# Kernel optimization log

Hardware: AMD Instinct MI355X
Metric: run time of the kernel (lower is better)

## Reference

```python
import jax, jax.numpy as jnp
import numpy as np

B, T, SD = 16, 512, 64          # batch, action seq len, sample_dim
EMB, HD = 1024, 64              # emb_dim, head_dim
NH = EMB // HD                  # 16 heads
DEPTH, NREG, LAT, FF = 8, 16, 256, 4 * EMB
S = T + NREG                    # total sequence length (actions + registers)


def setup_inputs() -> dict:
    key = jax.random.key(0)
    ks = jax.random.split(key, 16)
    def n(k, shape, scale=0.02):
        return jax.random.normal(k, shape, jnp.float32) * scale
    return {
        "sample": jax.random.normal(ks[0], (B, T, SD), jnp.float32),
        "W_emb": n(ks[1], (SD, EMB)), "b_emb": jnp.zeros((EMB,), jnp.float32),
        "pos": n(ks[2], (T, EMB)),
        "registers": n(ks[3], (NREG, EMB), 1.0),
        "ln1_s": jnp.ones((DEPTH, EMB), jnp.float32), "ln1_b": jnp.zeros((DEPTH, EMB), jnp.float32),
        "W_qkv": n(ks[4], (DEPTH, EMB, 3 * EMB)), "b_qkv": jnp.zeros((DEPTH, 3 * EMB), jnp.float32),
        "W_o": n(ks[5], (DEPTH, EMB, EMB)), "b_o": jnp.zeros((DEPTH, EMB), jnp.float32),
        "ln2_s": jnp.ones((DEPTH, EMB), jnp.float32), "ln2_b": jnp.zeros((DEPTH, EMB), jnp.float32),
        "W_fc1": n(ks[6], (DEPTH, EMB, FF)), "b_fc1": jnp.zeros((DEPTH, FF), jnp.float32),
        "W_fc2": n(ks[7], (DEPTH, FF, EMB)), "b_fc2": jnp.zeros((DEPTH, EMB), jnp.float32),
        "lnf_s": jnp.ones((EMB,), jnp.float32), "lnf_b": jnp.zeros((EMB,), jnp.float32),
        "W_head": n(ks[8], (EMB, LAT)), "b_head": jnp.zeros((LAT,), jnp.float32),
    }


def _ln(x, s, b):
    m = jnp.mean(x, -1, keepdims=True)
    v = jnp.var(x, -1, keepdims=True)
    return (x - m) * jax.lax.rsqrt(v + 1e-5) * s + b


def _causal_last_mask():
    # True = attended to. Actions attend to all actions but NOT registers;
    # registers attend to all actions and causally (incl. self) to registers.
    allowed = jnp.ones((S, S), jnp.bool_)
    allowed = allowed.at[:T, T:].set(False)
    allowed = allowed.at[T:, T:].set(jnp.tril(jnp.ones((NREG, NREG), jnp.bool_)))
    return allowed


def reference(sample, W_emb, b_emb, pos, registers, ln1_s, ln1_b, W_qkv, b_qkv,
              W_o, b_o, ln2_s, ln2_b, W_fc1, b_fc1, W_fc2, b_fc2,
              lnf_s, lnf_b, W_head, b_head):
    # embed + positional add
    x = sample @ W_emb + b_emb + pos[None, :, :]          # [B,T,E]
    # concat registers
    x = jnp.concatenate([x, jnp.broadcast_to(registers, (B, NREG, EMB))], axis=1)  # [B,S,E]
    mask = _causal_last_mask()                             # [S,S]
    scale = 1.0 / jnp.sqrt(jnp.asarray(HD, x.dtype))
    for i in range(DEPTH):
        # pre-LN multi-head attention with structured block mask
        h = _ln(x, ln1_s[i], ln1_b[i])
        qkv = h @ W_qkv[i] + b_qkv[i]
        q, k, v = jnp.split(qkv, 3, axis=-1)
        q = q.reshape(B, S, NH, HD)
        k = k.reshape(B, S, NH, HD)
        v = v.reshape(B, S, NH, HD)
        att = jnp.einsum('bqhd,bkhd->bhqk', q, k) * scale
        att = jnp.where(mask[None, None], att, jnp.finfo(att.dtype).min)
        att = jax.nn.softmax(att, axis=-1)
        o = jnp.einsum('bhqk,bkhd->bqhd', att, v).reshape(B, S, EMB)
        x = x + o @ W_o[i] + b_o[i]
        # pre-LN MLP
        h2 = _ln(x, ln2_s[i], ln2_b[i])
        x = x + jax.nn.gelu(h2 @ W_fc1[i] + b_fc1[i]) @ W_fc2[i] + b_fc2[i]
    x = _ln(x, lnf_s, lnf_b)
    # head applied to register positions only
    return x[:, T:] @ W_head + b_head                      # [B,NREG,LAT]
```

## Files before the change

kernel.cpp:

```cpp
#include <hip/hip_runtime.h>
#include <hip/hip_bf16.h>


typedef unsigned short u16;
typedef __attribute__((ext_vector_type(4))) float f32x4;
typedef __attribute__((ext_vector_type(8))) __bf16 bf16x8;

#define DEV static __device__ __forceinline__

constexpr int Bb = 16, Tt = 512, E = 1024, HD = 64, NHd = 16;
constexpr int DEPTH = 8, NREG = 16, LAT = 256, FF = 4096;
constexpr int S = Tt + NREG;
constexpr int SPAD = 576;
constexpr int MR = Bb * S;
constexpr int ME = Bb * Tt;

DEV u16 f2bf(float f) {
  unsigned u = __builtin_bit_cast(unsigned, f);
  u += 0x7fffu + ((u >> 16) & 1u);
  return (u16)(u >> 16);
}
DEV float bf2f(u16 h) { return __builtin_bit_cast(float, (unsigned)h << 16); }

DEV void gll16(const u16* g, u16* l) {
  __builtin_amdgcn_global_load_lds((const __attribute__((address_space(1))) void*)g,
                                   (__attribute__((address_space(3))) void*)l, 16, 0, 0);
}

enum { M_EMBED, M_QKV, M_OPROJ, M_FC1, M_FC2, M_HEAD };

struct GA {
  const u16* A; const u16* Bt;
  int K, lda, ldb, Nrows, ldc;
  const float* bias; const float* pos;
  float* fout; u16* bout;
  u16 *qp, *kp, *vtp;
};

template<int MODE, int BN>
__global__ __launch_bounds__(256)
void gemm_bt(GA g) {
  constexpr int NI = BN / 32;
  __shared__ __align__(16) u16 As[3][128 * 32];
  __shared__ __align__(16) u16 Bs[3][BN * 32];
  const int tid = threadIdx.x;
  const u16* A  = g.A;
  const u16* Bt = g.Bt;

  int tM, tN;
  {
    const int nwg = gridDim.x * gridDim.y;
    int flat = blockIdx.y * gridDim.x + blockIdx.x;
    const int q = nwg >> 3, r = nwg & 7;
    const int xcd = flat & 7, loc = flat >> 3;
    flat = (xcd < r ? xcd * (q + 1) : r * (q + 1) + (xcd - r) * q) + loc;
    tM = flat / gridDim.x; tN = flat % gridDim.x;
  }

  const int lane = tid & 63, wid = tid >> 6;
  const int wr = wid >> 1, wc = wid & 1;
  const int fr = lane & 15, fg = lane >> 4;

  const int arow = tM * 128 + (tid >> 2);
  int br0 = tN * BN + (tid >> 2);
  if (br0 > g.Nrows - 1) br0 = g.Nrows - 1;
  int br1 = tN * BN + 64 + (tid >> 2);
  if (br1 > g.Nrows - 1) br1 = g.Nrows - 1;
  const int kseg = ((tid & 3) ^ ((tid >> 3) & 3)) * 8;
  const int woff = (tid & 192) * 8;

  const u16* ag0 = A  + (long)arow        * g.lda + kseg;
  const u16* ag1 = A  + (long)(arow + 64) * g.lda + kseg;
  const u16* bg0 = Bt + (long)br0         * g.ldb + kseg;
  const u16* bg1 = Bt + (long)br1         * g.ldb + kseg;

  f32x4 acc[4][NI];
#pragma unroll
  for (int i = 0; i < 4; ++i)
#pragma unroll
    for (int j = 0; j < NI; ++j) acc[i][j] = f32x4{0.f, 0.f, 0.f, 0.f};

#define STAGE(KT, BUF) do {                                   \
    const int _k0 = (KT) << 5;                                \
    gll16(ag0 + _k0, &As[BUF][woff]);                         \
    gll16(ag1 + _k0, &As[BUF][woff + 2048]);                  \
    gll16(bg0 + _k0, &Bs[BUF][woff]);                         \
    if (BN == 128) gll16(bg1 + _k0, &Bs[BUF][woff + 2048]);   \
  } while (0)

  const int nk = g.K >> 5;
  STAGE(0, 0);
  if (nk > 1) STAGE(1, 1);

  const int rsw = (fg ^ ((fr >> 1) & 3)) * 8;
  constexpr int LPS = (BN == 128) ? 4 : 3;

  for (int kt = 0; kt < nk; ++kt) {
    const int cur = kt % 3;
    if (kt < nk - 1) {
      asm volatile("s_waitcnt vmcnt(%0)" :: "i"(LPS) : "memory");
    } else {
      asm volatile("s_waitcnt vmcnt(0)" ::: "memory");
    }
    __builtin_amdgcn_sched_barrier(0);
    __builtin_amdgcn_s_barrier();
    __builtin_amdgcn_sched_barrier(0);
    if (kt + 2 < nk) STAGE(kt + 2, (kt + 2) % 3);

    bf16x8 af[4], bfr[NI];
#pragma unroll
    for (int mi = 0; mi < 4; ++mi)
      af[mi] = *(const bf16x8*)&As[cur][(wr * 64 + mi * 16 + fr) * 32 + rsw];
#pragma unroll
    for (int ni = 0; ni < NI; ++ni)
      bfr[ni] = *(const bf16x8*)&Bs[cur][(wc * (BN / 2) + ni * 16 + fr) * 32 + rsw];
    __builtin_amdgcn_s_setprio(1);
#pragma unroll
    for (int mi = 0; mi < 4; ++mi)
#pragma unroll
      for (int ni = 0; ni < NI; ++ni)
        acc[mi][ni] = __builtin_amdgcn_mfma_f32_16x16x32_bf16(af[mi], bfr[ni], acc[mi][ni], 0, 0, 0);
    __builtin_amdgcn_s_setprio(0);
  }
#undef STAGE

#pragma unroll
  for (int mi = 0; mi < 4; ++mi)
#pragma unroll
    for (int ni = 0; ni < NI; ++ni)
#pragma unroll
      for (int j = 0; j < 4; ++j) {
        const int row = tM * 128 + wr * 64 + mi * 16 + fg * 4 + j;
        const int col = tN * BN + wc * (BN / 2) + ni * 16 + fr;
        float v = acc[mi][ni][j];
        if (MODE == M_EMBED) {
          const int b = row >> 9, t = row & 511;
          v += g.bias[col] + g.pos[(long)t * E + col];
          g.fout[((long)(b * S + t)) * E + col] = v;
        } else if (MODE == M_QKV) {
          const int b = row / S, s = row - b * S;
          v += g.bias[col];
          const int part = col >> 10, c = col & 1023;
          const int hh = c >> 6, d = c & 63;
          const u16 bf = f2bf(v);
          if (part == 0)      g.qp [((long)((b * NHd + hh) * SPAD + s)) * HD + d] = bf;
          else if (part == 1) g.kp [((long)((b * NHd + hh) * SPAD + s)) * HD + d] = bf;
          else                g.vtp[((long)((b * NHd + hh) * HD   + d)) * SPAD + s] = bf;
        } else if (MODE == M_OPROJ || MODE == M_FC2) {
          const long idx = (long)row * g.ldc + col;
          g.fout[idx] += v + g.bias[col];
        } else if (MODE == M_FC1) {
          v += g.bias[col];
          const float z = 0.7978845608028654f * (v + 0.044715f * v * v * v);
          const float e = __expf(2.f * z);
          const float th = 1.f - 2.f / (e + 1.f);
          g.bout[(long)row * g.ldc + col] = f2bf(0.5f * v * (1.f + th));
        } else if (MODE == M_HEAD) {
          g.fout[(long)row * g.ldc + col] = v + g.bias[col];
        }
      }
}

__global__ __launch_bounds__(256)
void flash_k(const u16* __restrict__ q, const u16* __restrict__ k,
             const u16* __restrict__ vt, u16* __restrict__ o) {
  __shared__ __align__(16) u16 Ks[2][64 * 64];
  __shared__ __align__(16) u16 Vs[2][64 * 64];
  __shared__ __align__(16) u16 Ps[4 * 32 * 64];
  const int tid = threadIdx.x;
  const int lane = tid & 63, w = tid >> 6;
  const int fr = lane & 15, fg = lane >> 4;

  int flat = blockIdx.y * 5 + blockIdx.x;
  flat = (flat & 7) * 160 + (flat >> 3);
  const int bh = flat / 5, qt = flat % 5;
  const int q0 = qt * 128;

  bf16x8 qf[2][2];
#pragma unroll
  for (int ms = 0; ms < 2; ++ms) {
    int qr = q0 + w * 32 + ms * 16 + fr;
    if (qr > SPAD - 1) qr = SPAD - 1;
    const u16* qrow = q + ((long)bh * SPAD + qr) * HD;
    qf[ms][0] = *(const bf16x8*)(qrow + fg * 8);
    qf[ms][1] = *(const bf16x8*)(qrow + 32 + fg * 8);
  }

  const int srow = lane >> 3;
  const int sseg = (((lane & 7) ^ (srow & 7)) * 8);
  const u16* kg = k  + ((long)bh * SPAD + w * 16 + srow) * HD + sseg;
  const u16* vg = vt + ((long)(bh * HD + w * 16 + srow)) * SPAD + sseg;

#define STAGE_F(KT, BUF) do {                                       \
    gll16(kg + (KT) * 64 * HD,          &Ks[BUF][w * 16 * HD]);     \
    gll16(kg + (KT) * 64 * HD + 8 * HD, &Ks[BUF][w * 16 * HD + 8 * HD]); \
    gll16(vg + (KT) * 64,               &Vs[BUF][w * 16 * HD]);     \
    gll16(vg + (KT) * 64 + 8 * SPAD,    &Vs[BUF][w * 16 * HD + 8 * HD]); \
  } while (0)

  const int frm = fr & 7;

  float m[2][4], lsum[2][4]; f32x4 oa[2][4];
#pragma unroll
  for (int ms = 0; ms < 2; ++ms)
#pragma unroll
    for (int j = 0; j < 4; ++j) { m[ms][j] = -1e30f; lsum[ms][j] = 0.f; }
#pragma unroll
  for (int ms = 0; ms < 2; ++ms)
#pragma unroll
    for (int n = 0; n < 4; ++n) oa[ms][n] = f32x4{0.f, 0.f, 0.f, 0.f};

  const int nt = (qt < 4) ? 8 : 9;
  STAGE_F(0, 0);
  for (int kt = 0; kt < nt; ++kt) {
    const int cur = kt & 1;
    asm volatile("s_waitcnt vmcnt(0)" ::: "memory");
    __builtin_amdgcn_sched_barrier(0);
    __builtin_amdgcn_s_barrier();
    __builtin_amdgcn_sched_barrier(0);
    if (kt + 1 < nt) STAGE_F(kt + 1, cur ^ 1);

    f32x4 sfr[2][4];
#pragma unroll
    for (int n = 0; n < 4; ++n) {
      const bf16x8 kf0 = *(const bf16x8*)&Ks[cur][(n * 16 + fr) * HD + ((fg ^ frm) * 8)];
      const bf16x8 kf1 = *(const bf16x8*)&Ks[cur][(n * 16 + fr) * HD + (((fg + 4) ^ frm) * 8)];
#pragma unroll
      for (int ms = 0; ms < 2; ++ms) {
        sfr[ms][n] = __builtin_amdgcn_mfma_f32_16x16x32_bf16(qf[ms][0], kf0, f32x4{0.f,0.f,0.f,0.f}, 0, 0, 0);
        sfr[ms][n] = __builtin_amdgcn_mfma_f32_16x16x32_bf16(qf[ms][1], kf1, sfr[ms][n], 0, 0, 0);
      }
    }
    float p[2][4][4];
#pragma unroll
    for (int ms = 0; ms < 2; ++ms)
#pragma unroll
      for (int j = 0; j < 4; ++j) {
        const int qg = q0 + w * 32 + ms * 16 + fg * 4 + j;
        const int vlim = qg < Tt ? Tt : qg + 1;
#pragma unroll
        for (int n = 0; n < 4; ++n) {
          const int col = kt * 64 + n * 16 + fr;
          p[ms][n][j] = (col < vlim) ? sfr[ms][n][j] * 0.125f : -1e30f;
        }
      }
#pragma unroll
    for (int ms = 0; ms < 2; ++ms)
#pragma unroll
      for (int j = 0; j < 4; ++j) {
        float pm = fmaxf(fmaxf(p[ms][0][j], p[ms][1][j]), fmaxf(p[ms][2][j], p[ms][3][j]));
#pragma unroll
        for (int msk = 1; msk <= 8; msk <<= 1) pm = fmaxf(pm, __shfl_xor(pm, msk));
        const float mn = fmaxf(m[ms][j], pm);
        const float corr = __expf(m[ms][j] - mn);
        m[ms][j] = mn;
        float rs = 0.f;
#pragma unroll
        for (int n = 0; n < 4; ++n) { const float e = __expf(p[ms][n][j] - mn); p[ms][n][j] = e; rs += e; }
#pragma unroll
        for (int msk = 1; msk <= 8; msk <<= 1) rs += __shfl_xor(rs, msk);
        lsum[ms][j] = lsum[ms][j] * corr + rs;
#pragma unroll
        for (int n = 0; n < 4; ++n) oa[ms][n][j] *= corr;
      }
#pragma unroll
    for (int ms = 0; ms < 2; ++ms)
#pragma unroll
      for (int j = 0; j < 4; ++j) {
        const int r = ms * 16 + fg * 4 + j;
#pragma unroll
        for (int n = 0; n < 4; ++n) {
          const int gr = 2 * n + (fr >> 3);
          Ps[w * 2048 + r * 64 + ((gr ^ (r & 7)) * 8) + frm] = f2bf(p[ms][n][j]);
        }
      }
    asm volatile("s_waitcnt lgkmcnt(0)" ::: "memory");
    __builtin_amdgcn_sched_barrier(0);
    bf16x8 pf[2][2];
#pragma unroll
    for (int ms = 0; ms < 2; ++ms) {
      pf[ms][0] = *(const bf16x8*)&Ps[w * 2048 + (ms * 16 + fr) * 64 + ((fg ^ frm) * 8)];
      pf[ms][1] = *(const bf16x8*)&Ps[w * 2048 + (ms * 16 + fr) * 64 + (((fg + 4) ^ frm) * 8)];
    }
#pragma unroll
    for (int n = 0; n < 4; ++n) {
      const bf16x8 vf0 = *(const bf16x8*)&Vs[cur][(n * 16 + fr) * HD + ((fg ^ frm) * 8)];
      const bf16x8 vf1 = *(const bf16x8*)&Vs[cur][(n * 16 + fr) * HD + (((fg + 4) ^ frm) * 8)];
#pragma unroll
      for (int ms = 0; ms < 2; ++ms) {
        oa[ms][n] = __builtin_amdgcn_mfma_f32_16x16x32_bf16(pf[ms][0], vf0, oa[ms][n], 0, 0, 0);
        oa[ms][n] = __builtin_amdgcn_mfma_f32_16x16x32_bf16(pf[ms][1], vf1, oa[ms][n], 0, 0, 0);
      }
    }
  }
#undef STAGE_F

  const int b = bh >> 4, hh = bh & 15;
#pragma unroll
  for (int ms = 0; ms < 2; ++ms)
#pragma unroll
    for (int j = 0; j < 4; ++j) {
      const int qg = q0 + w * 32 + ms * 16 + fg * 4 + j;
      if (qg < S) {
        const float inv = 1.f / lsum[ms][j];
#pragma unroll
        for (int n = 0; n < 4; ++n)
          o[((long)(b * S + qg)) * E + hh * HD + n * 16 + fr] = f2bf(oa[ms][n][j] * inv);
      }
    }
}

__global__ __launch_bounds__(256)
void ln_k(const float* __restrict__ x, const float* __restrict__ sc,
          const float* __restrict__ bi, u16* __restrict__ out, int gather) {
  const int r = blockIdx.x;
  const int srow = gather ? ((r >> 4) * S + Tt + (r & 15)) : r;
  const float4 v = ((const float4*)(x + (long)srow * E))[threadIdx.x];
  float s = v.x + v.y + v.z + v.w;
  float q = v.x * v.x + v.y * v.y + v.z * v.z + v.w * v.w;
#pragma unroll
  for (int o = 32; o; o >>= 1) { s += __shfl_down(s, o); q += __shfl_down(q, o); }
  __shared__ float ps[8];
  if ((threadIdx.x & 63) == 0) { ps[threadIdx.x >> 6] = s; ps[4 + (threadIdx.x >> 6)] = q; }
  __syncthreads();
  s = ps[0] + ps[1] + ps[2] + ps[3];
  q = ps[4] + ps[5] + ps[6] + ps[7];
  const float mean = s * (1.f / E);
  const float rs = rsqrtf(q * (1.f / E) - mean * mean + 1e-5f);
  const int c = threadIdx.x * 4;
  ushort4 o4;
  o4.x = f2bf((v.x - mean) * rs * sc[c + 0] + bi[c + 0]);
  o4.y = f2bf((v.y - mean) * rs * sc[c + 1] + bi[c + 1]);
  o4.z = f2bf((v.z - mean) * rs * sc[c + 2] + bi[c + 2]);
  o4.w = f2bf((v.w - mean) * rs * sc[c + 3] + bi[c + 3]);
  ((ushort4*)(out + (long)r * E))[threadIdx.x] = o4;
}

__global__ __launch_bounds__(256)
void wtrans(const float* __restrict__ src, u16* __restrict__ dst, int R, int C) {
  __shared__ float t[32][33];
  const int c0 = blockIdx.x * 32, r0 = blockIdx.y * 32;
  const int tx = threadIdx.x & 31, ty = threadIdx.x >> 5;
#pragma unroll
  for (int i = 0; i < 32; i += 8) t[ty + i][tx] = src[(long)(r0 + ty + i) * C + c0 + tx];
  __syncthreads();
#pragma unroll
  for (int i = 0; i < 32; i += 8) dst[(long)(c0 + ty + i) * R + r0 + tx] = f2bf(t[tx][ty + i]);
}

struct WT4 {
  const float* s[4]; u16* d[4];
  int R[4], C[4], tx[4], st[4];
};
__global__ __launch_bounds__(256)
void wtrans4(WT4 a) {
  const int bid = blockIdx.x;
  const int wsel = (bid >= a.st[1]) + (bid >= a.st[2]) + (bid >= a.st[3]);
  const int t = bid - a.st[wsel];
  const int c0 = (t % a.tx[wsel]) * 32, r0 = (t / a.tx[wsel]) * 32;
  const float* src = a.s[wsel]; u16* dst = a.d[wsel];
  const int R = a.R[wsel], C = a.C[wsel];
  __shared__ float tt[32][33];
  const int tx = threadIdx.x & 31, ty = threadIdx.x >> 5;
#pragma unroll
  for (int i = 0; i < 32; i += 8) tt[ty + i][tx] = src[(long)(r0 + ty + i) * C + c0 + tx];
  __syncthreads();
#pragma unroll
  for (int i = 0; i < 32; i += 8) dst[(long)(c0 + ty + i) * R + r0 + tx] = f2bf(tt[tx][ty + i]);
}

__global__ void cvt_bf(const float* __restrict__ in, u16* __restrict__ out, long n) {
  const long i = ((long)blockIdx.x * blockDim.x + threadIdx.x) * 4;
  if (i >= n) return;
  const float4 v = *(const float4*)(in + i);
  ushort4 o; o.x = f2bf(v.x); o.y = f2bf(v.y); o.z = f2bf(v.z); o.w = f2bf(v.w);
  *(ushort4*)(out + i) = o;
}

__global__ void zero_k(float4* p, long n) {
  long i = (long)blockIdx.x * blockDim.x + threadIdx.x;
  const long st = (long)gridDim.x * blockDim.x;
  const float4 z = make_float4(0.f, 0.f, 0.f, 0.f);
  for (; i < n; i += st) p[i] = z;
}

__global__ void reg_copy(const float* __restrict__ regs, float* __restrict__ x) {
  const int b = blockIdx.x >> 4, r = blockIdx.x & 15;
  const float4* sp = (const float4*)(regs + (long)r * E);
  float4* dp = (float4*)(x + ((long)(b * S + Tt + r)) * E);
  dp[threadIdx.x] = sp[threadIdx.x];
}

constexpr long OFF_WQKV = 0L;
constexpr long OFF_WO   = OFF_WQKV + 3072L * 1024 * 2;
constexpr long OFF_WFC1 = OFF_WO   + 1024L * 1024 * 2;
constexpr long OFF_WFC2 = OFF_WFC1 + 4096L * 1024 * 2;
constexpr long OFF_WEMB = OFF_WFC2 + 1024L * 4096 * 2;
constexpr long OFF_WHEAD= OFF_WEMB + 1024L * 64 * 2;
constexpr long OFF_SMP  = OFF_WHEAD+ 256L * 1024 * 2;
constexpr long OFF_X    = OFF_SMP  + (long)ME * 64 * 2;
constexpr long OFF_H    = OFF_X    + (long)MR * E * 4;
constexpr long OFF_Q    = OFF_H    + (long)MR * E * 2;
constexpr long OFF_K    = OFF_Q    + 256L * SPAD * HD * 2;
constexpr long OFF_VT   = OFF_K    + 256L * SPAD * HD * 2;
constexpr long OFF_O    = OFF_VT   + 256L * SPAD * HD * 2;
constexpr long OFF_HF   = OFF_O    + (long)MR * FF * 2;
constexpr long WS_NEED  = OFF_HF   + 256L * 1024 * 2;

extern "C" void kernel_launch(void* const* d_in, const int* in_sizes, int n_in,
                              void* d_out, int out_size, void* d_ws, size_t ws_size,
                              hipStream_t stream) {
  if (ws_size < (size_t)WS_NEED) return;

  const float* sample = (const float*)d_in[0];
  const float* W_emb  = (const float*)d_in[1];
  const float* b_emb  = (const float*)d_in[2];
  const float* pos    = (const float*)d_in[3];
  const float* regs   = (const float*)d_in[4];
  const float* ln1_s  = (const float*)d_in[5];
  const float* ln1_b  = (const float*)d_in[6];
  const float* W_qkv  = (const float*)d_in[7];
  const float* b_qkv  = (const float*)d_in[8];
  const float* W_o    = (const float*)d_in[9];
  const float* b_o    = (const float*)d_in[10];
  const float* ln2_s  = (const float*)d_in[11];
  const float* ln2_b  = (const float*)d_in[12];
  const float* W_fc1  = (const float*)d_in[13];
  const float* b_fc1  = (const float*)d_in[14];
  const float* W_fc2  = (const float*)d_in[15];
  const float* b_fc2  = (const float*)d_in[16];
  const float* lnf_s  = (const float*)d_in[17];
  const float* lnf_b  = (const float*)d_in[18];
  const float* W_head = (const float*)d_in[19];
  const float* b_head = (const float*)d_in[20];

  char* w = (char*)d_ws;
  u16* wqkvT = (u16*)(w + OFF_WQKV);
  u16* woT   = (u16*)(w + OFF_WO);
  u16* wfc1T = (u16*)(w + OFF_WFC1);
  u16* wfc2T = (u16*)(w + OFF_WFC2);
  u16* wembT = (u16*)(w + OFF_WEMB);
  u16* wheadT= (u16*)(w + OFF_WHEAD);
  u16* smp   = (u16*)(w + OFF_SMP);
  float* x   = (float*)(w + OFF_X);
  u16* h     = (u16*)(w + OFF_H);
  u16* qp    = (u16*)(w + OFF_Q);
  u16* kp    = (u16*)(w + OFF_K);
  u16* vtp   = (u16*)(w + OFF_VT);
  u16* o     = (u16*)(w + OFF_O);
  u16* a1    = (u16*)(w + OFF_O);
  u16* hf    = (u16*)(w + OFF_HF);

  wtrans<<<dim3(32, 2, 1), 256, 0, stream>>>(W_emb,  wembT, 64, 1024);
  wtrans<<<dim3(8, 32, 1), 256, 0, stream>>>(W_head, wheadT, 1024, 256);
  cvt_bf<<<dim3(512), 256, 0, stream>>>(sample, smp, (long)ME * 64);
  zero_k<<<dim3(2048), 256, 0, stream>>>((float4*)qp, (3L * 256 * SPAD * HD * 2) / 16);

  {
    GA g{}; g.A = smp; g.Bt = wembT; g.K = 64; g.lda = 64; g.ldb = 64;
    g.Nrows = E; g.bias = b_emb; g.pos = pos; g.fout = x;
    gemm_bt<M_EMBED, 64><<<dim3(16, 64, 1), 256, 0, stream>>>(g);
  }
  reg_copy<<<dim3(256), 256, 0, stream>>>(regs, x);

  for (int L = 0; L < DEPTH; ++L) {
    {
      WT4 a;
      a.s[0] = W_qkv + (long)L * 1024 * 3072; a.d[0] = wqkvT; a.R[0] = 1024; a.C[0] = 3072; a.tx[0] = 96;  a.st[0] = 0;
      a.s[1] = W_o   + (long)L * 1024 * 1024; a.d[1] = woT;   a.R[1] = 1024; a.C[1] = 1024; a.tx[1] = 32;  a.st[1] = 3072;
      a.s[2] = W_fc1 + (long)L * 1024 * 4096; a.d[2] = wfc1T; a.R[2] = 1024; a.C[2] = 4096; a.tx[2] = 128; a.st[2] = 4096;
      a.s[3] = W_fc2 + (long)L * 4096 * 1024; a.d[3] = wfc2T; a.R[3] = 4096; a.C[3] = 1024; a.tx[3] = 32;  a.st[3] = 8192;
      wtrans4<<<dim3(12288), 256, 0, stream>>>(a);
    }

    ln_k<<<dim3(MR), 256, 0, stream>>>(x, ln1_s + L * E, ln1_b + L * E, h, 0);
    {
      GA g{}; g.A = h; g.Bt = wqkvT;
      g.K = 1024; g.lda = 1024; g.ldb = 1024; g.Nrows = 3072;
      g.bias = b_qkv + L * 3072; g.qp = qp; g.kp = kp; g.vtp = vtp;
      gemm_bt<M_QKV, 128><<<dim3(24, 66, 1), 256, 0, stream>>>(g);
    }
    flash_k<<<dim3(5, 256, 1), 256, 0, stream>>>(qp, kp, vtp, o);
    {
      GA g{}; g.A = o; g.Bt = woT;
      g.K = 1024; g.lda = 1024; g.ldb = 1024; g.Nrows = 1024; g.ldc = 1024;
      g.bias = b_o + L * E; g.fout = x;
      gemm_bt<M_OPROJ, 128><<<dim3(8, 66, 1), 256, 0, stream>>>(g);
    }
    ln_k<<<dim3(MR), 256, 0, stream>>>(x, ln2_s + L * E, ln2_b + L * E, h, 0);
    {
      GA g{}; g.A = h; g.Bt = wfc1T;
      g.K = 1024; g.lda = 1024; g.ldb = 1024; g.Nrows = 4096; g.ldc = 4096;
      g.bias = b_fc1 + L * FF; g.bout = a1;
      gemm_bt<M_FC1, 128><<<dim3(32, 66, 1), 256, 0, stream>>>(g);
    }
    {
      GA g{}; g.A = a1; g.Bt = wfc2T;
      g.K = 4096; g.lda = 4096; g.ldb = 4096; g.Nrows = 1024; g.ldc = 1024;
      g.bias = b_fc2 + L * E; g.fout = x;
      gemm_bt<M_FC2, 128><<<dim3(8, 66, 1), 256, 0, stream>>>(g);
    }
  }

  ln_k<<<dim3(256), 256, 0, stream>>>(x, lnf_s, lnf_b, hf, 1);
  {
    GA g{}; g.A = hf; g.Bt = wheadT; g.K = 1024; g.lda = 1024; g.ldb = 1024;
    g.Nrows = LAT; g.ldc = LAT; g.bias = b_head; g.fout = (float*)d_out;
    gemm_bt<M_HEAD, 128><<<dim3(2, 2, 1), 256, 0, stream>>>(g);
  }
}
```

Before: 3.886 ms.

## Load GEMM B operand directly from global into registers, bypassing LDS

```diff
diff --git a/kernel.cpp b/kernel.cpp
--- a/kernel.cpp
+++ b/kernel.cpp
@@ -42,7 +42,6 @@
 void gemm_bt(GA g) {
   constexpr int NI = BN / 32;
   __shared__ __align__(16) u16 As[3][128 * 32];
-  __shared__ __align__(16) u16 Bs[3][BN * 32];
   const int tid = threadIdx.x;
   const u16* A  = g.A;
   const u16* Bt = g.Bt;
@@ -62,17 +61,11 @@
   const int fr = lane & 15, fg = lane >> 4;
 
   const int arow = tM * 128 + (tid >> 2);
-  int br0 = tN * BN + (tid >> 2);
-  if (br0 > g.Nrows - 1) br0 = g.Nrows - 1;
-  int br1 = tN * BN + 64 + (tid >> 2);
-  if (br1 > g.Nrows - 1) br1 = g.Nrows - 1;
   const int kseg = ((tid & 3) ^ ((tid >> 3) & 3)) * 8;
   const int woff = (tid & 192) * 8;
-
-  const u16* ag0 = A  + (long)arow        * g.lda + kseg;
-  const u16* ag1 = A  + (long)(arow + 64) * g.lda + kseg;
-  const u16* bg0 = Bt + (long)br0         * g.ldb + kseg;
-  const u16* bg1 = Bt + (long)br1         * g.ldb + kseg;
+  const u16* ag0 = A + (long)arow        * g.lda + kseg;
+  const u16* ag1 = A + (long)(arow + 64) * g.lda + kseg;
+  const u16* bp = Bt + (long)(tN * BN + wc * (BN / 2) + fr) * g.ldb + fg * 8;
 
   f32x4 acc[4][NI];
 #pragma unroll
@@ -80,49 +73,73 @@
 #pragma unroll
     for (int j = 0; j < NI; ++j) acc[i][j] = f32x4{0.f, 0.f, 0.f, 0.f};
 
-#define STAGE(KT, BUF) do {                                   \
+#define STAGE_A(KT, BUF) do {                                 \
     const int _k0 = (KT) << 5;                                \
     gll16(ag0 + _k0, &As[BUF][woff]);                         \
     gll16(ag1 + _k0, &As[BUF][woff + 2048]);                  \
-    gll16(bg0 + _k0, &Bs[BUF][woff]);                         \
-    if (BN == 128) gll16(bg1 + _k0, &Bs[BUF][woff + 2048]);   \
   } while (0)
+#define LOADB(DST, KT) do {                                   \
+    _Pragma("unroll")                                         \
+    for (int ni = 0; ni < NI; ++ni)                           \
+      DST[ni] = *(const bf16x8*)(bp + (long)ni * 16 * g.ldb + ((KT) << 5)); \
+  } while (0)
 
   const int nk = g.K >> 5;
-  STAGE(0, 0);
-  if (nk > 1) STAGE(1, 1);
+  STAGE_A(0, 0);
+  if (nk > 1) STAGE_A(1, 1);
+  bf16x8 bA[NI], bB[NI];
+  LOADB(bA, 0);
 
   const int rsw = (fg ^ ((fr >> 1) & 3)) * 8;
-  constexpr int LPS = (BN == 128) ? 4 : 3;
-
-  for (int kt = 0; kt < nk; ++kt) {
-    const int cur = kt % 3;
-    if (kt < nk - 1) {
-      asm volatile("s_waitcnt vmcnt(%0)" :: "i"(LPS) : "memory");
-    } else {
-      asm volatile("s_waitcnt vmcnt(0)" ::: "memory");
-    }
-    __builtin_amdgcn_sched_barrier(0);
-    __builtin_amdgcn_s_barrier();
-    __builtin_amdgcn_sched_barrier(0);
-    if (kt + 2 < nk) STAGE(kt + 2, (kt + 2) % 3);
-
-    bf16x8 af[4], bfr[NI];
-#pragma unroll
-    for (int mi = 0; mi < 4; ++mi)
-      af[mi] = *(const bf16x8*)&As[cur][(wr * 64 + mi * 16 + fr) * 32 + rsw];
-#pragma unroll
-    for (int ni = 0; ni < NI; ++ni)
-      bfr[ni] = *(const bf16x8*)&Bs[cur][(wc * (BN / 2) + ni * 16 + fr) * 32 + rsw];
-    __builtin_amdgcn_s_setprio(1);
-#pragma unroll
-    for (int mi = 0; mi < 4; ++mi)
-#pragma unroll
-      for (int ni = 0; ni < NI; ++ni)
-        acc[mi][ni] = __builtin_amdgcn_mfma_f32_16x16x32_bf16(af[mi], bfr[ni], acc[mi][ni], 0, 0, 0);
-    __builtin_amdgcn_s_setprio(0);
-  }
-#undef STAGE
+
+  for (int kt = 0; kt < nk; kt += 2) {
+    {
+      const int cur = kt % 3;
+      asm volatile("s_waitcnt vmcnt(%0)" :: "i"(2 + NI) : "memory");
+      __builtin_amdgcn_sched_barrier(0);
+      __builtin_amdgcn_s_barrier();
+      __builtin_amdgcn_sched_barrier(0);
+      if (kt + 2 < nk) STAGE_A(kt + 2, (kt + 2) % 3);
+      LOADB(bB, kt + 1);
+      bf16x8 af[4];
+#pragma unroll
+      for (int mi = 0; mi < 4; ++mi)
+        af[mi] = *(const bf16x8*)&As[cur][(wr * 64 + mi * 16 + fr) * 32 + rsw];
+      __builtin_amdgcn_s_setprio(1);
+#pragma unroll
+      for (int mi = 0; mi < 4; ++mi)
+#pragma unroll
+        for (int ni = 0; ni < NI; ++ni)
+          acc[mi][ni] = __builtin_amdgcn_mfma_f32_16x16x32_bf16(af[mi], bA[ni], acc[mi][ni], 0, 0, 0);
+      __builtin_amdgcn_s_setprio(0);
+    }
+    {
+      const int cur = (kt + 1) % 3;
+      if (kt + 1 < nk - 1) {
+        asm volatile("s_waitcnt vmcnt(%0)" :: "i"(2 + NI) : "memory");
+      } else {
+        asm volatile("s_waitcnt vmcnt(%0)" :: "i"(NI) : "memory");
+      }
+      __builtin_amdgcn_sched_barrier(0);
+      __builtin_amdgcn_s_barrier();
+      __builtin_amdgcn_sched_barrier(0);
+      if (kt + 3 < nk) STAGE_A(kt + 3, (kt + 3) % 3);
+      if (kt + 2 < nk) LOADB(bA, kt + 2);
+      bf16x8 af[4];
+#pragma unroll
+      for (int mi = 0; mi < 4; ++mi)
+        af[mi] = *(const bf16x8*)&As[cur][(wr * 64 + mi * 16 + fr) * 32 + rsw];
+      __builtin_amdgcn_s_setprio(1);
+#pragma unroll
+      for (int mi = 0; mi < 4; ++mi)
+#pragma unroll
+        for (int ni = 0; ni < NI; ++ni)
+          acc[mi][ni] = __builtin_amdgcn_mfma_f32_16x16x32_bf16(af[mi], bB[ni], acc[mi][ni], 0, 0, 0);
+      __builtin_amdgcn_s_setprio(0);
+    }
+  }
+#undef STAGE_A
+#undef LOADB
 
 #pragma unroll
   for (int mi = 0; mi < 4; ++mi)
```

Result: slower. 5.892 ms (+51.6%).

## Add 8-wave 256x128-tile GEMM kernel for transformer layer matmuls

Applied to the files above, without the earlier changes.

```diff
diff --git a/kernel.cpp b/kernel.cpp
--- a/kernel.cpp
+++ b/kernel.cpp
@@ -36,6 +36,35 @@
   float* fout; u16* bout;
   u16 *qp, *kp, *vtp;
 };
+
+template<int MODE>
+DEV void epilogue(const GA& g, int row, int col, float v) {
+  if (MODE == M_EMBED) {
+    const int b = row >> 9, t = row & 511;
+    v += g.bias[col] + g.pos[(long)t * E + col];
+    g.fout[((long)(b * S + t)) * E + col] = v;
+  } else if (MODE == M_QKV) {
+    const int b = row / S, s = row - b * S;
+    v += g.bias[col];
+    const int part = col >> 10, c = col & 1023;
+    const int hh = c >> 6, d = c & 63;
+    const u16 bf = f2bf(v);
+    if (part == 0)      g.qp [((long)((b * NHd + hh) * SPAD + s)) * HD + d] = bf;
+    else if (part == 1) g.kp [((long)((b * NHd + hh) * SPAD + s)) * HD + d] = bf;
+    else                g.vtp[((long)((b * NHd + hh) * HD   + d)) * SPAD + s] = bf;
+  } else if (MODE == M_OPROJ || MODE == M_FC2) {
+    const long idx = (long)row * g.ldc + col;
+    g.fout[idx] += v + g.bias[col];
+  } else if (MODE == M_FC1) {
+    v += g.bias[col];
+    const float z = 0.7978845608028654f * (v + 0.044715f * v * v * v);
+    const float e = __expf(2.f * z);
+    const float th = 1.f - 2.f / (e + 1.f);
+    g.bout[(long)row * g.ldc + col] = f2bf(0.5f * v * (1.f + th));
+  } else if (MODE == M_HEAD) {
+    g.fout[(long)row * g.ldc + col] = v + g.bias[col];
+  }
+}
 
 template<int MODE, int BN>
 __global__ __launch_bounds__(256)
@@ -129,36 +158,92 @@
 #pragma unroll
     for (int ni = 0; ni < NI; ++ni)
 #pragma unroll
-      for (int j = 0; j < 4; ++j) {
-        const int row = tM * 128 + wr * 64 + mi * 16 + fg * 4 + j;
-        const int col = tN * BN + wc * (BN / 2) + ni * 16 + fr;
-        float v = acc[mi][ni][j];
-        if (MODE == M_EMBED) {
-          const int b = row >> 9, t = row & 511;
-          v += g.bias[col] + g.pos[(long)t * E + col];
-          g.fout[((long)(b * S + t)) * E + col] = v;
-        } else if (MODE == M_QKV) {
-          const int b = row / S, s = row - b * S;
-          v += g.bias[col];
-          const int part = col >> 10, c = col & 1023;
-          const int hh = c >> 6, d = c & 63;
-          const u16 bf = f2bf(v);
-          if (part == 0)      g.qp [((long)((b * NHd + hh) * SPAD + s)) * HD + d] = bf;
-          else if (part == 1) g.kp [((long)((b * NHd + hh) * SPAD + s)) * HD + d] = bf;
-          else                g.vtp[((long)((b * NHd + hh) * HD   + d)) * SPAD + s] = bf;
-        } else if (MODE == M_OPROJ || MODE == M_FC2) {
-          const long idx = (long)row * g.ldc + col;
-          g.fout[idx] += v + g.bias[col];
-        } else if (MODE == M_FC1) {
-          v += g.bias[col];
-          const float z = 0.7978845608028654f * (v + 0.044715f * v * v * v);
-          const float e = __expf(2.f * z);
-          const float th = 1.f - 2.f / (e + 1.f);
-          g.bout[(long)row * g.ldc + col] = f2bf(0.5f * v * (1.f + th));
-        } else if (MODE == M_HEAD) {
-          g.fout[(long)row * g.ldc + col] = v + g.bias[col];
-        }
-      }
+      for (int j = 0; j < 4; ++j)
+        epilogue<MODE>(g, tM * 128 + wr * 64 + mi * 16 + fg * 4 + j,
+                       tN * BN + wc * (BN / 2) + ni * 16 + fr, acc[mi][ni][j]);
+}
+
+template<int MODE>
+__global__ __launch_bounds__(512)
+void gemm_w8(GA g) {
+  __shared__ __align__(16) u16 As[3][256 * 32];
+  __shared__ __align__(16) u16 Bs[3][128 * 32];
+  const int tid = threadIdx.x;
+
+  int tM, tN;
+  {
+    const int nwg = gridDim.x * gridDim.y;
+    int flat = blockIdx.y * gridDim.x + blockIdx.x;
+    const int q = nwg >> 3, r = nwg & 7;
+    const int xcd = flat & 7, loc = flat >> 3;
+    flat = (xcd < r ? xcd * (q + 1) : r * (q + 1) + (xcd - r) * q) + loc;
+    tM = flat / gridDim.x; tN = flat % gridDim.x;
+  }
+
+  const int lane = tid & 63, wid = tid >> 6;
+  const int wr = wid >> 1, wc = wid & 1;
+  const int fr = lane & 15, fg = lane >> 4;
+
+  const int kseg = ((lane & 3) ^ ((lane >> 3) & 3)) * 8;
+  const u16* ag = g.A  + (long)(tM * 256 + wid * 32 + (lane >> 2)) * g.lda + kseg;
+  const u16* bg = g.Bt + (long)(tN * 128 + wid * 16 + (lane >> 2)) * g.ldb + kseg;
+
+  f32x4 acc[4][4];
+#pragma unroll
+  for (int i = 0; i < 4; ++i)
+#pragma unroll
+    for (int j = 0; j < 4; ++j) acc[i][j] = f32x4{0.f, 0.f, 0.f, 0.f};
+
+#define STAGE8(KT, BUF) do {                                        \
+    const int _k0 = (KT) << 5;                                      \
+    gll16(ag + _k0,                 &As[BUF][wid * 1024]);          \
+    gll16(ag + (long)16 * g.lda + _k0, &As[BUF][wid * 1024 + 512]); \
+    gll16(bg + _k0,                 &Bs[BUF][wid * 512]);           \
+  } while (0)
+
+  const int nk = g.K >> 5;
+  STAGE8(0, 0);
+  STAGE8(1, 1);
+
+  const int rsw = (fg ^ ((fr >> 1) & 3)) * 8;
+
+  for (int kt = 0; kt < nk; ++kt) {
+    const int cur = kt % 3;
+    if (kt < nk - 1) {
+      asm volatile("s_waitcnt vmcnt(3)" ::: "memory");
+    } else {
+      asm volatile("s_waitcnt vmcnt(0)" ::: "memory");
+    }
+    __builtin_amdgcn_sched_barrier(0);
+    __builtin_amdgcn_s_barrier();
+    __builtin_amdgcn_sched_barrier(0);
+    if (kt + 2 < nk) STAGE8(kt + 2, (kt + 2) % 3);
+
+    bf16x8 af[4], bfr[4];
+#pragma unroll
+    for (int mi = 0; mi < 4; ++mi)
+      af[mi] = *(const bf16x8*)&As[cur][(wr * 64 + mi * 16 + fr) * 32 + rsw];
+#pragma unroll
+    for (int ni = 0; ni < 4; ++ni)
+      bfr[ni] = *(const bf16x8*)&Bs[cur][(wc * 64 + ni * 16 + fr) * 32 + rsw];
+    __builtin_amdgcn_s_setprio(1);
+#pragma unroll
+    for (int mi = 0; mi < 4; ++mi)
+#pragma unroll
+      for (int ni = 0; ni < 4; ++ni)
+        acc[mi][ni] = __builtin_amdgcn_mfma_f32_16x16x32_bf16(af[mi], bfr[ni], acc[mi][ni], 0, 0, 0);
+    __builtin_amdgcn_s_setprio(0);
+  }
+#undef STAGE8
+
+#pragma unroll
+  for (int mi = 0; mi < 4; ++mi)
+#pragma unroll
+    for (int ni = 0; ni < 4; ++ni)
+#pragma unroll
+      for (int j = 0; j < 4; ++j)
+        epilogue<MODE>(g, tM * 256 + wr * 64 + mi * 16 + fg * 4 + j,
+                       tN * 128 + wc * 64 + ni * 16 + fr, acc[mi][ni][j]);
 }
 
 __global__ __launch_bounds__(256)
@@ -478,27 +563,27 @@
       GA g{}; g.A = h; g.Bt = wqkvT;
       g.K = 1024; g.lda = 1024; g.ldb = 1024; g.Nrows = 3072;
       g.bias = b_qkv + L * 3072; g.qp = qp; g.kp = kp; g.vtp = vtp;
-      gemm_bt<M_QKV, 128><<<dim3(24, 66, 1), 256, 0, stream>>>(g);
+      gemm_w8<M_QKV><<<dim3(24, 33, 1), 512, 0, stream>>>(g);
     }
     flash_k<<<dim3(5, 256, 1), 256, 0, stream>>>(qp, kp, vtp, o);
     {
       GA g{}; g.A = o; g.Bt = woT;
       g.K = 1024; g.lda = 1024; g.ldb = 1024; g.Nrows = 1024; g.ldc = 1024;
       g.bias = b_o + L * E; g.fout = x;
-      gemm_bt<M_OPROJ, 128><<<dim3(8, 66, 1), 256, 0, stream>>>(g);
+      gemm_w8<M_OPROJ><<<dim3(8, 33, 1), 512, 0, stream>>>(g);
     }
     ln_k<<<dim3(MR), 256, 0, stream>>>(x, ln2_s + L * E, ln2_b + L * E, h, 0);
     {
       GA g{}; g.A = h; g.Bt = wfc1T;
       g.K = 1024; g.lda = 1024; g.ldb = 1024; g.Nrows = 4096; g.ldc = 4096;
       g.bias = b_fc1 + L * FF; g.bout = a1;
-      gemm_bt<M_FC1, 128><<<dim3(32, 66, 1), 256, 0, stream>>>(g);
+      gemm_w8<M_FC1><<<dim3(32, 33, 1), 512, 0, stream>>>(g);
     }
     {
       GA g{}; g.A = a1; g.Bt = wfc2T;
       g.K = 4096; g.lda = 4096; g.ldb = 4096; g.Nrows = 1024; g.ldc = 1024;
       g.bias = b_fc2 + L * E; g.fout = x;
-      gemm_bt<M_FC2, 128><<<dim3(8, 66, 1), 256, 0, stream>>>(g);
+      gemm_w8<M_FC2><<<dim3(8, 33, 1), 512, 0, stream>>>(g);
     }
   }
 
```

New measurement: 4.207 ms. 1.08x slower.
